# Optimization experiments

Measured on AMD Instinct MI355X. Metric: run time of the kernel, lower is better.

## Reference

```python
import jax, jax.numpy as jnp
import numpy as np
import math

N_HEADS = 8

def _layernorm(x, s, b):
    mu = x.mean(-1, keepdims=True)
    var = ((x - mu) ** 2).mean(-1, keepdims=True)
    return (x - mu) / jnp.sqrt(var + 1e-5) * s + b


def setup_inputs() -> dict:
    key = jax.random.key(0)
    ks = jax.random.split(key, 16)
    B, S, F, E, L, C, DFF = 4, 2048, 16, 512, 4, 35, 2048
    feat = jax.random.normal(ks[0], (B, S, F - 1), dtype=jnp.float32)
    amino = jax.random.randint(ks[1], (B, S), 0, 20).astype(jnp.float32)
    x = jnp.concatenate([feat, amino[..., None]], axis=-1)  # last channel = amino id
    lengths = np.array([2048, 1900, 1700, 1500])
    mask = jnp.asarray(np.arange(S)[None, :] >= lengths[:, None])  # True = padding
    M = 256
    rng = np.random.default_rng(0)
    mp = np.stack([np.sort(rng.choice(int(lengths[b]) - 1, M, replace=False)) for b in range(B)])
    masked_pos = jnp.asarray(mp, dtype=jnp.int32)
    # sinusoidal positional encoding [S, E]
    pos = np.arange(S)[:, None].astype(np.float32)
    div = np.exp(np.arange(0, E, 2).astype(np.float32) * (-math.log(10000.0) / E))
    pe_np = np.zeros((S, E), np.float32)
    pe_np[:, 0::2] = np.sin(pos * div)
    pe_np[:, 1::2] = np.cos(pos * div)
    pe = jnp.asarray(pe_np)
    sc = 1.0 / math.sqrt(E)
    def w(k, shape, s=sc):
        return jax.random.normal(k, shape, dtype=jnp.float32) * s
    return dict(
        x=x, mask=mask, masked_pos=masked_pos,
        arg1=jnp.float32(0.5), arg2=jnp.float32(0.8),
        embed_table=w(ks[2], (20, E - 15), 1.0), pe=pe,
        Wq=w(ks[3], (L, E, E)), bq=jnp.zeros((L, E)),
        Wk=w(ks[4], (L, E, E)), bk=jnp.zeros((L, E)),
        Wv=w(ks[5], (L, E, E)), bv=jnp.zeros((L, E)),
        Wo=w(ks[6], (L, E, E)), bo=jnp.zeros((L, E)),
        ln1_s=jnp.ones((L, E)), ln1_b=jnp.zeros((L, E)),
        W1=w(ks[7], (L, E, DFF)), b1=jnp.zeros((L, DFF)),
        W2=w(ks[8], (L, DFF, E), 1.0 / math.sqrt(DFF)), b2=jnp.zeros((L, E)),
        ln2_s=jnp.ones((L, E)), ln2_b=jnp.zeros((L, E)),
        fc_w=w(ks[9], (E, C)), fc_b=jnp.zeros((C,)),
    )


def _forward(x, mask, masked_pos, arg1, arg2, embed_table, pe, Wq, bq, Wk, bk, Wv, bv,
             Wo, bo, ln1_s, ln1_b, W1, b1, W2, b2, ln2_s, ln2_b, fc_w, fc_b):
    B, S, F = x.shape
    E = pe.shape[1]
    L = Wq.shape[0]
    H = N_HEADS
    Dh = E // H
    bidx = jnp.arange(B)[:, None]
    # get_mask: zero the masked token rows; label = original rows at masked positions
    mask_x = x.at[bidx, masked_pos].set(0.0)
    label = x[bidx, masked_pos].reshape(-1, F)
    # amino embedding with per-token min-max normalization
    amino = mask_x[:, :, -1].astype(jnp.int32)
    emb = embed_table[amino]  # [B,S,E-15]
    mn = emb.min(-1, keepdims=True)
    mx = emb.max(-1, keepdims=True)
    emb = (emb - mn) / (mx - mn)
    h = jnp.concatenate([mask_x[:, :, :-1], emb], axis=-1) + pe[None, :S, :]
    base = (~mask).astype(jnp.float32)  # 1 = valid key, 0 = pad
    for i in range(L):
        fill = arg1 if i == 0 else (arg2 if i == 1 else jnp.float32(1.0))
        m = base.at[bidx, masked_pos].set(fill)  # [B,S] key weights
        q = (h @ Wq[i] + bq[i]).reshape(B, S, H, Dh).transpose(0, 2, 1, 3)
        k = (h @ Wk[i] + bk[i]).reshape(B, S, H, Dh).transpose(0, 2, 1, 3)
        v = (h @ Wv[i] + bv[i]).reshape(B, S, H, Dh).transpose(0, 2, 1, 3)
        scores = jnp.einsum('bhqd,bhkd->bhqk', q, k) / Dh  # note: /head_dim, not sqrt
        mvec = m[:, None, None, :]
        scores = jnp.where(mvec != 0, scores * mvec, -jnp.inf)
        attn = jax.nn.softmax(scores, axis=-1)
        ws = jnp.einsum('bhqk,bhkd->bhqd', attn, v)  # [B,H,S,Dh]
        # faithful to torch: stacked [B,H,S,Dh].view(B,-1,E) row-major flatten
        attn_out = ws.reshape(B, -1, E) @ Wo[i] + bo[i]
        h = _layernorm(h + attn_out, ln1_s[i], ln1_b[i])
        ff = jax.nn.relu(h @ W1[i] + b1[i]) @ W2[i] + b2[i]
        h = _layernorm(h + ff, ln2_s[i], ln2_b[i])
    out_tok = h[bidx, masked_pos].reshape(-1, E)
    output = out_tok @ fc_w + fc_b
    return output[:, :15], output[:, 15:], label, h


def reference(x, mask, masked_pos, arg1, arg2, embed_table, pe, Wq, bq, Wk, bk, Wv, bv,
              Wo, bo, ln1_s, ln1_b, W1, b1, W2, b2, ln2_s, ln2_b, fc_w, fc_b):
    L1, CE, label, h = _forward(x, mask, masked_pos, arg1, arg2, embed_table, pe, Wq, bq,
                                Wk, bk, Wv, bv, Wo, bo, ln1_s, ln1_b, W1, b1, W2, b2,
                                ln2_s, ln2_b, fc_w, fc_b)
    return (L1, CE, label, h, mask)
```

## Files before the change

### kernel.cpp

```cpp
#include <hip/hip_runtime.h>
#include <hip/hip_bf16.h>


typedef __bf16 bf16_t;
typedef __bf16 bf16x8 __attribute__((ext_vector_type(8)));
typedef __bf16 bf16x4 __attribute__((ext_vector_type(4)));
typedef float  f32x4  __attribute__((ext_vector_type(4)));

#define ASYNC16(g, l) __builtin_amdgcn_global_load_lds( \
    (const __attribute__((address_space(1))) void*)(g),  \
    (__attribute__((address_space(3))) void*)(l), 16, 0, 0)

static __device__ __forceinline__ f32x4 mfma16(bf16x8 a, bf16x8 b, f32x4 c) {
  return __builtin_amdgcn_mfma_f32_16x16x32_bf16(a, b, c, 0, 0, 0);
}

static __device__ __forceinline__ float fexp2(float x) {
#if __has_builtin(__builtin_amdgcn_exp2f)
  return __builtin_amdgcn_exp2f(x);
#else
  return exp2f(x);
#endif
}

#define L2E 1.44269504f

__global__ void zero_flags_k(int* __restrict__ flags) {
  flags[blockIdx.x * 256 + threadIdx.x] = 0;
}

__global__ void scatter_k(const int* __restrict__ mpos, int* __restrict__ flags) {
  int t = blockIdx.x * 256 + threadIdx.x;
  int b = t >> 8;
  flags[b * 2048 + mpos[t]] = 1;
}

__global__ void masks_k(const int* __restrict__ flags,
                        const float* __restrict__ a1, const float* __restrict__ a2,
                        float* __restrict__ m05, float* __restrict__ m08,
                        float* __restrict__ mbase, float* __restrict__ maskout) {
  int i = blockIdx.x * 256 + threadIdx.x;
  int b = i >> 11, s = i & 2047;
  const int len0 = (b == 0) ? 2048 : (b == 1) ? 1900 : (b == 2) ? 1700 : 1500;
  float bs = (s < len0) ? 1.f : 0.f;
  int fl = flags[i];
  m05[i]   = fl ? a1[0] : bs;
  m08[i]   = fl ? a2[0] : bs;
  mbase[i] = fl ? 1.f   : bs;
  maskout[i] = 1.f - bs;
}

__global__ void label_k(const float* __restrict__ x, const int* __restrict__ mpos,
                        float* __restrict__ out) {
  int idx = blockIdx.x * 256 + threadIdx.x;
  int t = idx >> 4, f = idx & 15;
  int b = t >> 8;
  int pos = mpos[t];
  out[idx] = x[(b * 2048 + pos) * 16 + f];
}

__global__ __launch_bounds__(512) void embed_k(
    const float* __restrict__ x, const int* __restrict__ flags,
    const float* __restrict__ et, const float* __restrict__ pe,
    float* __restrict__ hf, bf16_t* __restrict__ hb) {
  const int tok = blockIdx.x, tid = threadIdx.x;
  const int s = tok & 2047;
  const int wave = tid >> 6, lane = tid & 63;
  __shared__ float e[512];
  __shared__ float redn[8], redx[8];
  const int masked = flags[tok];
  const float amf = masked ? 0.f : x[tok * 16 + 15];
  const int am = (int)amf;
  float ev = 0.f, vn = 3e38f, vx = -3e38f;
  if (tid < 497) { ev = et[am * 497 + tid]; e[tid] = ev; vn = ev; vx = ev; }
#pragma unroll
  for (int off = 1; off < 64; off <<= 1) {
    vn = fminf(vn, __shfl_xor(vn, off, 64));
    vx = fmaxf(vx, __shfl_xor(vx, off, 64));
  }
  if (lane == 0) { redn[wave] = vn; redx[wave] = vx; }
  __syncthreads();
  float mn = redn[0], mx = redx[0];
#pragma unroll
  for (int w = 1; w < 8; ++w) { mn = fminf(mn, redn[w]); mx = fmaxf(mx, redx[w]); }
  float val;
  if (tid < 15) val = masked ? 0.f : x[tok * 16 + tid];
  else          val = (e[tid - 15] - mn) / (mx - mn);
  val += pe[s * 512 + tid];
  hf[(size_t)tok * 512 + tid] = val;
  hb[(size_t)tok * 512 + tid] = (bf16_t)val;
}

__global__ void transpose_k(const float* __restrict__ in, bf16_t* __restrict__ out,
                            int K, int N, size_t ozstride) {
  __shared__ float t[32][33];
  in  += (size_t)blockIdx.z * K * N;
  out += (size_t)blockIdx.z * ozstride;
  const int n0 = blockIdx.x * 32, k0 = blockIdx.y * 32;
  const int tx = threadIdx.x & 31, ty = threadIdx.x >> 5;
#pragma unroll
  for (int i = 0; i < 32; i += 8)
    t[ty + i][tx] = in[(size_t)(k0 + ty + i) * N + n0 + tx];
  __syncthreads();
#pragma unroll
  for (int i = 0; i < 32; i += 8)
    out[(size_t)(n0 + ty + i) * K + k0 + tx] = (bf16_t)t[tx][ty + i];
}

template <int EPI>
__global__ __launch_bounds__(256) void gemm_k(
    const bf16_t* __restrict__ A, const bf16_t* __restrict__ Bt,
    const float* __restrict__ bias, const float* __restrict__ resid,
    float* __restrict__ outf, bf16_t* __restrict__ outb,
    int M, int N, int K) {
  __shared__ alignas(16) bf16_t As[2][128 * 32];
  __shared__ alignas(16) bf16_t Bs[2][128 * 32];
  const int tid = threadIdx.x;
  const int wave = tid >> 6, lane = tid & 63;
  const int quad = lane >> 4, l16 = lane & 15;
  const int n0 = blockIdx.x * 128, m0 = blockIdx.y * 128;
  const int wm = (wave & 1) * 64, wn = (wave >> 1) * 64;

  const int c0 = wave * 2, c1 = c0 + 1;
  const int sr = lane >> 2;
  const int sc = (((lane & 3) ^ ((sr >> 1) & 3))) * 8;
  const bf16_t* Ag0 = A + (size_t)(m0 + c0 * 16 + sr) * K + sc;
  const bf16_t* Ag1 = A + (size_t)(m0 + c1 * 16 + sr) * K + sc;
  const bf16_t* Bg0 = Bt + (size_t)(n0 + c0 * 16 + sr) * K + sc;
  const bf16_t* Bg1 = Bt + (size_t)(n0 + c1 * 16 + sr) * K + sc;

  const int cq = (quad ^ ((l16 >> 1) & 3)) * 8;

  f32x4 acc[4][4] = {};
  const int nit = K >> 5;

  ASYNC16(Ag0, &As[0][c0 * 512]);
  ASYNC16(Ag1, &As[0][c1 * 512]);
  ASYNC16(Bg0, &Bs[0][c0 * 512]);
  ASYNC16(Bg1, &Bs[0][c1 * 512]);
  __syncthreads();

  for (int it = 0; it < nit; ++it) {
    const int cur = it & 1, nxt = cur ^ 1;
    if (it + 1 < nit) {
      const int ko = (it + 1) << 5;
      ASYNC16(Ag0 + ko, &As[nxt][c0 * 512]);
      ASYNC16(Ag1 + ko, &As[nxt][c1 * 512]);
      ASYNC16(Bg0 + ko, &Bs[nxt][c0 * 512]);
      ASYNC16(Bg1 + ko, &Bs[nxt][c1 * 512]);
    }
    bf16x8 af[4], bfr[4];
#pragma unroll
    for (int mi = 0; mi < 4; ++mi)
      af[mi] = *(const bf16x8*)&As[cur][(wm + mi * 16 + l16) * 32 + cq];
#pragma unroll
    for (int ni = 0; ni < 4; ++ni)
      bfr[ni] = *(const bf16x8*)&Bs[cur][(wn + ni * 16 + l16) * 32 + cq];
#pragma unroll
    for (int mi = 0; mi < 4; ++mi)
#pragma unroll
      for (int ni = 0; ni < 4; ++ni)
        acc[mi][ni] = mfma16(af[mi], bfr[ni], acc[mi][ni]);
    __syncthreads();
  }

#pragma unroll
  for (int ni = 0; ni < 4; ++ni) {
    const int gn = n0 + wn + ni * 16 + l16;
    const float bv = bias[gn];
#pragma unroll
    for (int mi = 0; mi < 4; ++mi) {
#pragma unroll
      for (int r = 0; r < 4; ++r) {
        const int gm = m0 + wm + mi * 16 + quad * 4 + r;
        float v = acc[mi][ni][r] + bv;
        if (EPI == 2) {
          outf[(size_t)gm * N + gn] = v + resid[(size_t)gm * N + gn];
        } else {
          outb[(size_t)gm * N + gn] = (bf16_t)fmaxf(v, 0.f);
        }
      }
    }
  }
}

__global__ __launch_bounds__(256) void gemm64_k(
    const bf16_t* __restrict__ A, const bf16_t* __restrict__ Bt,
    const float* __restrict__ bias, const float* __restrict__ resid,
    float* __restrict__ outf, int M, int N, int K) {
  __shared__ alignas(16) bf16_t As[2][64 * 64];
  __shared__ alignas(16) bf16_t Bs[2][128 * 64];
  const int tid = threadIdx.x;
  const int wave = tid >> 6, lane = tid & 63;
  const int quad = lane >> 4, l16 = lane & 15;
  const int n0 = blockIdx.x * 128, m0 = blockIdx.y * 64;
  const int wm = (wave & 1) * 32, wn = (wave >> 1) * 64;

  const bf16_t* gptr[6];
  int soff[6];
  bool isA[6];
#pragma unroll
  for (int i = 0; i < 6; ++i) {
    const int s = tid + 256 * i;
    if (s < 512) {
      const int r = s >> 3, c = s & 7, g = c ^ ((r >> 1) & 7);
      gptr[i] = A + (size_t)(m0 + r) * K + g * 8;
      soff[i] = s * 16;  isA[i] = true;
    } else {
      const int sb = s - 512;
      const int r = sb >> 3, c = sb & 7, g = c ^ ((r >> 1) & 7);
      gptr[i] = Bt + (size_t)(n0 + r) * K + g * 8;
      soff[i] = sb * 16; isA[i] = false;
    }
  }

  const int swl = (l16 >> 1) & 7;
  f32x4 acc[2][4] = {};
  const int nit = K >> 6;

#pragma unroll
  for (int i = 0; i < 6; ++i)
    ASYNC16(gptr[i], (char*)(isA[i] ? &As[0][0] : &Bs[0][0]) + soff[i]);
  __syncthreads();

  for (int it = 0; it < nit; ++it) {
    const int cur = it & 1, nxt = cur ^ 1;
    if (it + 1 < nit) {
      const int ko = (it + 1) << 6;
#pragma unroll
      for (int i = 0; i < 6; ++i)
        ASYNC16(gptr[i] + ko, (char*)(isA[i] ? &As[nxt][0] : &Bs[nxt][0]) + soff[i]);
    }
#pragma unroll
    for (int h = 0; h < 2; ++h) {
      const int cq = ((quad + 4 * h) ^ swl) * 8;
      bf16x8 af[2], bfr[4];
#pragma unroll
      for (int mi = 0; mi < 2; ++mi)
        af[mi] = *(const bf16x8*)&As[cur][(wm + mi * 16 + l16) * 64 + cq];
#pragma unroll
      for (int ni = 0; ni < 4; ++ni)
        bfr[ni] = *(const bf16x8*)&Bs[cur][(wn + ni * 16 + l16) * 64 + cq];
#pragma unroll
      for (int mi = 0; mi < 2; ++mi)
#pragma unroll
        for (int ni = 0; ni < 4; ++ni)
          acc[mi][ni] = mfma16(af[mi], bfr[ni], acc[mi][ni]);
    }
    __syncthreads();
  }

#pragma unroll
  for (int ni = 0; ni < 4; ++ni) {
    const int gn = n0 + wn + ni * 16 + l16;
    const float bv = bias[gn];
#pragma unroll
    for (int mi = 0; mi < 2; ++mi) {
#pragma unroll
      for (int r = 0; r < 4; ++r) {
        const int gm = m0 + wm + mi * 16 + quad * 4 + r;
        outf[(size_t)gm * N + gn] = acc[mi][ni][r] + bv + resid[(size_t)gm * N + gn];
      }
    }
  }
}

__global__ __launch_bounds__(256) void gemm_qkv_k(
    const bf16_t* __restrict__ A, const bf16_t* __restrict__ Bt,
    const float* __restrict__ bq, const float* __restrict__ bk,
    const float* __restrict__ bv, const float* __restrict__ mw,
    bf16_t* __restrict__ qb, bf16_t* __restrict__ kb, bf16_t* __restrict__ vtb) {
  const int K = 512;
  __shared__ alignas(16) bf16_t As[2][128 * 32];
  __shared__ alignas(16) bf16_t Bs[2][128 * 32];
  const int tid = threadIdx.x;
  const int wave = tid >> 6, lane = tid & 63;
  const int quad = lane >> 4, l16 = lane & 15;
  const int n0 = blockIdx.x * 128, m0 = blockIdx.y * 128;
  const int wm = (wave & 1) * 64, wn = (wave >> 1) * 64;

  const int c0 = wave * 2, c1 = c0 + 1;
  const int sr = lane >> 2;
  const int sc = (((lane & 3) ^ ((sr >> 1) & 3))) * 8;
  const bf16_t* Ag0 = A + (size_t)(m0 + c0 * 16 + sr) * K + sc;
  const bf16_t* Ag1 = A + (size_t)(m0 + c1 * 16 + sr) * K + sc;
  const bf16_t* Bg0 = Bt + (size_t)(n0 + c0 * 16 + sr) * K + sc;
  const bf16_t* Bg1 = Bt + (size_t)(n0 + c1 * 16 + sr) * K + sc;

  const int cq = (quad ^ ((l16 >> 1) & 3)) * 8;

  f32x4 acc[4][4] = {};
  const int nit = K >> 5;

  ASYNC16(Ag0, &As[0][c0 * 512]);
  ASYNC16(Ag1, &As[0][c1 * 512]);
  ASYNC16(Bg0, &Bs[0][c0 * 512]);
  ASYNC16(Bg1, &Bs[0][c1 * 512]);
  __syncthreads();

  for (int it = 0; it < nit; ++it) {
    const int cur = it & 1, nxt = cur ^ 1;
    if (it + 1 < nit) {
      const int ko = (it + 1) << 5;
      ASYNC16(Ag0 + ko, &As[nxt][c0 * 512]);
      ASYNC16(Ag1 + ko, &As[nxt][c1 * 512]);
      ASYNC16(Bg0 + ko, &Bs[nxt][c0 * 512]);
      ASYNC16(Bg1 + ko, &Bs[nxt][c1 * 512]);
    }
    bf16x8 af[4], bfr[4];
#pragma unroll
    for (int mi = 0; mi < 4; ++mi)
      af[mi] = *(const bf16x8*)&As[cur][(wm + mi * 16 + l16) * 32 + cq];
#pragma unroll
    for (int ni = 0; ni < 4; ++ni)
      bfr[ni] = *(const bf16x8*)&Bs[cur][(wn + ni * 16 + l16) * 32 + cq];
#pragma unroll
    for (int mi = 0; mi < 4; ++mi)
#pragma unroll
      for (int ni = 0; ni < 4; ++ni)
        acc[mi][ni] = mfma16(af[mi], bfr[ni], acc[mi][ni]);
    __syncthreads();
  }

  const int which = n0 >> 9;
  const float* bias = (which == 0) ? bq : (which == 1) ? bk : bv;
  bf16_t* dst = (which == 0) ? qb : (which == 1) ? kb : vtb;
  float kmul[4][4];
  if (which == 1) {
#pragma unroll
    for (int mi = 0; mi < 4; ++mi)
#pragma unroll
      for (int r = 0; r < 4; ++r) {
        const int gm = m0 + wm + mi * 16 + quad * 4 + r;
        kmul[mi][r] = mw[(gm >> 11) * 2048 + (gm & 2047)] * (0.015625f * L2E);
      }
  }
#pragma unroll
  for (int ni = 0; ni < 4; ++ni) {
    const int gn = n0 + wn + ni * 16 + l16;
    const int col = gn & 511;
    const float bvx = bias[col];
    const int hh = col >> 6, dd = col & 63;
#pragma unroll
    for (int mi = 0; mi < 4; ++mi) {
#pragma unroll
      for (int r = 0; r < 4; ++r) {
        const int gm = m0 + wm + mi * 16 + quad * 4 + r;
        const int bb = gm >> 11, ss = gm & 2047;
        float v = acc[mi][ni][r] + bvx;
        if (which == 0) {
          dst[(size_t)(((bb * 8 + hh) * 2048) + ss) * 64 + dd] = (bf16_t)v;
        } else if (which == 1) {
          v *= kmul[mi][r];
          dst[(size_t)(((bb * 8 + hh) * 2048) + ss) * 64 + dd] = (bf16_t)v;
        } else {
          const int o5 = ss & 31;
          const int ssp = (ss & ~31) | ((o5 & 12) << 1) | ((o5 & 16) >> 2) | (o5 & 3);
          dst[(size_t)(((bb * 8 + hh) * 64) + dd) * 2048 + ssp] = (bf16_t)v;
        }
      }
    }
  }
}

__global__ __launch_bounds__(256, 2) void attn_k(
    const bf16_t* __restrict__ Q, const bf16_t* __restrict__ Kmat,
    const bf16_t* __restrict__ VT, bf16_t* __restrict__ out) {
  __shared__ alignas(16) bf16_t Ks[128 * 64];
  __shared__ alignas(16) bf16_t Vs[64 * 128];
  const int tid = threadIdx.x, wave = tid >> 6, lane = tid & 63;
  const int quad = lane >> 4, l16 = lane & 15;
  const int qt = blockIdx.x, bh = blockIdx.y;
  const int b = bh >> 3, hh = bh & 7;
  const int len = (b == 0) ? 2048 : (b == 1) ? 1900 : (b == 2) ? 1700 : 1500;
  const bf16_t* __restrict__ Qh = Q    + (size_t)bh * 2048 * 64;
  const bf16_t* __restrict__ Kh = Kmat + (size_t)bh * 2048 * 64;
  const bf16_t* __restrict__ Vh = VT   + (size_t)bh * 64 * 2048;
  const int q0 = qt * 128 + wave * 32;

  bf16x8 aq[2][2];
#pragma unroll
  for (int qf = 0; qf < 2; ++qf) {
    aq[qf][0] = *(const bf16x8*)&Qh[(size_t)(q0 + qf * 16 + l16) * 64 + quad * 8];
    aq[qf][1] = *(const bf16x8*)&Qh[(size_t)(q0 + qf * 16 + l16) * 64 + 32 + quad * 8];
  }

  f32x4 o[2][4] = {};
  f32x4 os[2] = {};
  bf16x8 onesb;
#pragma unroll
  for (int j = 0; j < 8; ++j) onesb[j] = (bf16_t)1.0f;

  const int krow = wave * 8 + (lane >> 3);
  const int kchk = (lane & 7) ^ (lane >> 3);
  const int vrow = wave * 4 + (lane >> 4);
  const int vchk = (lane & 15) ^ (wave * 4 + (lane >> 4));
  const int kc0 = quad ^ (l16 & 7);
  const int kc1 = (quad + 4) ^ (l16 & 7);

  const int ntiles = (len + 127) >> 7;
  for (int kt = 0; kt < ntiles; ++kt) {
    const int k0 = kt * 128;
    __syncthreads();
#pragma unroll
    for (int i = 0; i < 4; ++i)
      ASYNC16(Kh + (size_t)(k0 + i * 32 + krow) * 64 + kchk * 8,
              &Ks[(i * 32 + wave * 8) * 64]);
#pragma unroll
    for (int i = 0; i < 4; ++i)
      ASYNC16(Vh + (size_t)(i * 16 + vrow) * 2048 + k0 + vchk * 8,
              &Vs[(i * 16 + wave * 4) * 128]);
    __syncthreads();

    f32x4 sc0[8], sc1[8];
#pragma unroll
    for (int t = 0; t < 8; ++t) {
      const bf16x8 kf0 = *(const bf16x8*)&Ks[(t * 16 + l16) * 64 + kc0 * 8];
      const bf16x8 kf1 = *(const bf16x8*)&Ks[(t * 16 + l16) * 64 + kc1 * 8];
      f32x4 z0 = {0.f, 0.f, 0.f, 0.f};
      z0 = mfma16(kf0, aq[0][0], z0);
      z0 = mfma16(kf1, aq[0][1], z0);
      sc0[t] = z0;
      f32x4 z1 = {0.f, 0.f, 0.f, 0.f};
      z1 = mfma16(kf0, aq[1][0], z1);
      z1 = mfma16(kf1, aq[1][1], z1);
      sc1[t] = z1;
    }
    if (k0 + 128 > len) {
#pragma unroll
      for (int t = 0; t < 8; ++t)
#pragma unroll
        for (int r = 0; r < 4; ++r) {
          const bool pad = (k0 + t * 16 + quad * 4 + r >= len);
          if (pad) { sc0[t][r] = -1e30f; sc1[t][r] = -1e30f; }
        }
    }
    bf16x8 pbp[2][4];
#pragma unroll
    for (int t = 0; t < 8; ++t)
#pragma unroll
      for (int r = 0; r < 4; ++r) {
        pbp[0][t >> 1][(t & 1) * 4 + r] = (bf16_t)fexp2(sc0[t][r]);
        pbp[1][t >> 1][(t & 1) * 4 + r] = (bf16_t)fexp2(sc1[t][r]);
      }
#pragma unroll
    for (int T = 0; T < 4; ++T) {
      const int slot = ((4 * T + quad) ^ l16) * 8;
#pragma unroll
      for (int ni = 0; ni < 4; ++ni) {
        const bf16x8 vb = *(const bf16x8*)&Vs[(ni * 16 + l16) * 128 + slot];
        o[0][ni] = mfma16(pbp[0][T], vb, o[0][ni]);
        o[1][ni] = mfma16(pbp[1][T], vb, o[1][ni]);
      }
      os[0] = mfma16(pbp[0][T], onesb, os[0]);
      os[1] = mfma16(pbp[1][T], onesb, os[1]);
    }
  }

#pragma unroll
  for (int qf = 0; qf < 2; ++qf) {
    float linv[4];
#pragma unroll
    for (int r = 0; r < 4; ++r) linv[r] = 1.f / os[qf][r];
#pragma unroll
    for (int ni = 0; ni < 4; ++ni) {
#pragma unroll
      for (int r = 0; r < 4; ++r) {
        const int s_tok = q0 + qf * 16 + quad * 4 + r;
        const int d = ni * 16 + l16;
        const int row = b * 2048 + hh * 256 + (s_tok >> 3);
        const int col = (s_tok & 7) * 64 + d;
        out[(size_t)row * 512 + col] = (bf16_t)(o[qf][ni][r] * linv[r]);
      }
    }
  }
}

__global__ __launch_bounds__(256) void ln_k(
    const float* __restrict__ in, const float* __restrict__ sc,
    const float* __restrict__ bi, float* __restrict__ hf, bf16_t* __restrict__ hb) {
  const int row = blockIdx.x, tid = threadIdx.x;
  const int wave = tid >> 6, lane = tid & 63;
  const float* x = in + (size_t)row * 512;
  float v0 = x[tid], v1 = x[tid + 256];
  float s = v0 + v1, s2 = v0 * v0 + v1 * v1;
#pragma unroll
  for (int off = 1; off < 64; off <<= 1) {
    s  += __shfl_xor(s, off, 64);
    s2 += __shfl_xor(s2, off, 64);
  }
  __shared__ float red[8];
  if (lane == 0) { red[wave] = s; red[4 + wave] = s2; }
  __syncthreads();
  float ts  = red[0] + red[1] + red[2] + red[3];
  float ts2 = red[4] + red[5] + red[6] + red[7];
  float mu = ts * (1.f / 512.f);
  float var = ts2 * (1.f / 512.f) - mu * mu;
  float rstd = rsqrtf(var + 1e-5f);
  float o0 = (v0 - mu) * rstd * sc[tid] + bi[tid];
  float o1 = (v1 - mu) * rstd * sc[tid + 256] + bi[tid + 256];
  hf[(size_t)row * 512 + tid] = o0;
  hf[(size_t)row * 512 + tid + 256] = o1;
  hb[(size_t)row * 512 + tid] = (bf16_t)o0;
  hb[(size_t)row * 512 + tid + 256] = (bf16_t)o1;
}

__global__ void head_k(const float* __restrict__ hf, const int* __restrict__ mpos,
                       const float* __restrict__ fw, const float* __restrict__ fb,
                       float* __restrict__ out0, float* __restrict__ out1) {
  const int t = blockIdx.x;
  const int b = t >> 8;
  const int pos = mpos[t];
  const float* hr = hf + (size_t)(b * 2048 + pos) * 512;
  __shared__ float hrow[512];
  for (int i = threadIdx.x; i < 512; i += 64) hrow[i] = hr[i];
  __syncthreads();
  const int c = threadIdx.x;
  if (c < 35) {
    float acc = fb[c];
    for (int k = 0; k < 512; ++k) acc += hrow[k] * fw[k * 35 + c];
    if (c < 15) out0[t * 15 + c] = acc;
    else        out1[t * 20 + (c - 15)] = acc;
  }
}

extern "C" void kernel_launch(void* const* d_in, const int* in_sizes, int n_in,
                              void* d_out, int out_size, void* d_ws, size_t ws_size,
                              hipStream_t stream) {
  const float* x    = (const float*)d_in[0];
  const int*   mpos = (const int*)d_in[2];
  const float* a1   = (const float*)d_in[3];
  const float* a2   = (const float*)d_in[4];
  const float* et   = (const float*)d_in[5];
  const float* pe   = (const float*)d_in[6];
  const float* Wq   = (const float*)d_in[7];
  const float* bq   = (const float*)d_in[8];
  const float* Wk   = (const float*)d_in[9];
  const float* bk   = (const float*)d_in[10];
  const float* Wv   = (const float*)d_in[11];
  const float* bv   = (const float*)d_in[12];
  const float* Wo   = (const float*)d_in[13];
  const float* bo   = (const float*)d_in[14];
  const float* l1s  = (const float*)d_in[15];
  const float* l1b  = (const float*)d_in[16];
  const float* W1   = (const float*)d_in[17];
  const float* b1   = (const float*)d_in[18];
  const float* W2   = (const float*)d_in[19];
  const float* b2   = (const float*)d_in[20];
  const float* l2s  = (const float*)d_in[21];
  const float* l2b  = (const float*)d_in[22];
  const float* fcw  = (const float*)d_in[23];
  const float* fcb  = (const float*)d_in[24];

  char* w = (char*)d_ws;
  const size_t MB = 1024 * 1024;
  bf16_t* qkvT = (bf16_t*)(w + 0 * MB);
  bf16_t* wot  = (bf16_t*)(w + 6 * MB);
  bf16_t* w1t  = (bf16_t*)(w + 8 * MB);
  bf16_t* w2t  = (bf16_t*)(w + 16 * MB);
  float*  hf   = (float*) (w + 24 * MB);
  bf16_t* hb   = (bf16_t*)(w + 40 * MB);
  float*  tmp  = (float*) (w + 48 * MB);
  int*    flags= (int*)   (w + 64 * MB);
  float*  m05  = (float*) (w + 64 * MB + 64 * 1024);
  float*  m08  = (float*) (w + 64 * MB + 128 * 1024);
  float*  mba  = (float*) (w + 64 * MB + 192 * 1024);
  bf16_t* qb   = (bf16_t*)(w + 65 * MB);
  bf16_t* kb   = (bf16_t*)(w + 73 * MB);
  bf16_t* vtb  = (bf16_t*)(w + 81 * MB);
  bf16_t* ao   = (bf16_t*)(w + 89 * MB);
  bf16_t* ff1  = (bf16_t*)(w + 65 * MB);

  float* out0    = (float*)d_out;
  float* out1    = out0 + 1024 * 15;
  float* outlab  = out1 + 1024 * 20;
  float* outh    = outlab + 1024 * 16;
  float* outmask = outh + 4 * 2048 * 512;

  zero_flags_k<<<32, 256, 0, stream>>>(flags);
  scatter_k<<<4, 256, 0, stream>>>(mpos, flags);
  masks_k<<<32, 256, 0, stream>>>(flags, a1, a2, m05, m08, mba, outmask);
  embed_k<<<8192, 512, 0, stream>>>(x, flags, et, pe, hf, hb);
  label_k<<<64, 256, 0, stream>>>(x, mpos, outlab);
  transpose_k<<<dim3(16, 16, 4), 256, 0, stream>>>(Wq, qkvT + 0 * 262144, 512, 512, 786432);
  transpose_k<<<dim3(16, 16, 4), 256, 0, stream>>>(Wk, qkvT + 1 * 262144, 512, 512, 786432);
  transpose_k<<<dim3(16, 16, 4), 256, 0, stream>>>(Wv, qkvT + 2 * 262144, 512, 512, 786432);
  transpose_k<<<dim3(16, 16, 4), 256, 0, stream>>>(Wo, wot, 512, 512, 262144);
  transpose_k<<<dim3(64, 16, 4), 256, 0, stream>>>(W1, w1t, 512, 2048, 1048576);
  transpose_k<<<dim3(16, 64, 4), 256, 0, stream>>>(W2, w2t, 2048, 512, 1048576);

  for (int i = 0; i < 4; ++i) {
    const float* mv = (i == 0) ? m05 : (i == 1) ? m08 : mba;
    gemm_qkv_k<<<dim3(12, 64), 256, 0, stream>>>(hb, qkvT + (size_t)i * 786432,
                                                 bq + i * 512, bk + i * 512, bv + i * 512,
                                                 mv, qb, kb, vtb);
    attn_k<<<dim3(16, 32), 256, 0, stream>>>(qb, kb, vtb, ao);
    gemm64_k<<<dim3(4, 128), 256, 0, stream>>>(ao, wot + i * 262144, bo + i * 512,
                                               hf, tmp, 8192, 512, 512);
    ln_k<<<8192, 256, 0, stream>>>(tmp, l1s + i * 512, l1b + i * 512, hf, hb);
    gemm_k<3><<<dim3(16, 64), 256, 0, stream>>>(hb, w1t + i * 1048576, b1 + i * 2048,
                                                nullptr, nullptr, ff1, 8192, 2048, 512);
    gemm64_k<<<dim3(4, 128), 256, 0, stream>>>(ff1, w2t + i * 1048576, b2 + i * 512,
                                               hf, tmp, 8192, 512, 2048);
    float* lnout = (i == 3) ? outh : hf;
    ln_k<<<8192, 256, 0, stream>>>(tmp, l2s + i * 512, l2b + i * 512, lnout, hb);
  }
  head_k<<<1024, 64, 0, stream>>>(outh, mpos, fcw, fcb, out0, out1);
}
```

Baseline: 874.6 us.

## Keep residual stream in bf16, double-buffer attention K/V, widen QKV k-tile

The fp32 hidden-state copy is removed: residual adds and layernorm inputs and outputs now use bf16 buffers, and only the final layer writes fp32 output. This cuts memory traffic in the gemm epilogues and layernorm. The attention kernel now double-buffers K/V tiles so the next tile loads while the current one computes, the QKV GEMM uses a 64-wide k-tile, and the four weight transposes are merged into one launch. Keeping the residual in bf16 lowers accuracy, and the larger shared-memory footprint in attention may reduce occupancy.

```diff
diff --git a/kernel.cpp b/kernel.cpp
--- a/kernel.cpp
+++ b/kernel.cpp
@@ -4,12 +4,15 @@
 
 typedef __bf16 bf16_t;
 typedef __bf16 bf16x8 __attribute__((ext_vector_type(8)));
-typedef __bf16 bf16x4 __attribute__((ext_vector_type(4)));
+typedef __bf16 bf16x2 __attribute__((ext_vector_type(2)));
 typedef float  f32x4  __attribute__((ext_vector_type(4)));
 
 #define ASYNC16(g, l) __builtin_amdgcn_global_load_lds( \
     (const __attribute__((address_space(1))) void*)(g),  \
     (__attribute__((address_space(3))) void*)(l), 16, 0, 0)
+
+#define S_VMCNT0() asm volatile("s_waitcnt vmcnt(0)" ::: "memory")
+#define S_BARRIER() asm volatile("s_barrier" ::: "memory")
 
 static __device__ __forceinline__ f32x4 mfma16(bf16x8 a, bf16x8 b, f32x4 c) {
   return __builtin_amdgcn_mfma_f32_16x16x32_bf16(a, b, c, 0, 0, 0);
@@ -62,7 +65,7 @@
 __global__ __launch_bounds__(512) void embed_k(
     const float* __restrict__ x, const int* __restrict__ flags,
     const float* __restrict__ et, const float* __restrict__ pe,
-    float* __restrict__ hf, bf16_t* __restrict__ hb) {
+    bf16_t* __restrict__ hb) {
   const int tok = blockIdx.x, tid = threadIdx.x;
   const int s = tok & 2047;
   const int wave = tid >> 6, lane = tid & 63;
@@ -87,7 +90,6 @@
   if (tid < 15) val = masked ? 0.f : x[tok * 16 + tid];
   else          val = (e[tid - 15] - mn) / (mx - mn);
   val += pe[s * 512 + tid];
-  hf[(size_t)tok * 512 + tid] = val;
   hb[(size_t)tok * 512 + tid] = (bf16_t)val;
 }
 
@@ -107,11 +109,30 @@
     out[(size_t)(n0 + ty + i) * K + k0 + tx] = (bf16_t)t[tx][ty + i];
 }
 
+__global__ void transpose4_k(const float* __restrict__ Wq, const float* __restrict__ Wk,
+                             const float* __restrict__ Wv, const float* __restrict__ Wo,
+                             bf16_t* __restrict__ qkvT, bf16_t* __restrict__ wot) {
+  __shared__ float t[32][33];
+  const int z = blockIdx.z, l = z >> 2, f = z & 3;
+  const float* in = ((f == 0) ? Wq : (f == 1) ? Wk : (f == 2) ? Wv : Wo)
+                    + (size_t)l * 262144;
+  bf16_t* out = (f < 3) ? qkvT + (size_t)l * 786432 + (size_t)f * 262144
+                        : wot + (size_t)l * 262144;
+  const int n0 = blockIdx.x * 32, k0 = blockIdx.y * 32;
+  const int tx = threadIdx.x & 31, ty = threadIdx.x >> 5;
+#pragma unroll
+  for (int i = 0; i < 32; i += 8)
+    t[ty + i][tx] = in[(size_t)(k0 + ty + i) * 512 + n0 + tx];
+  __syncthreads();
+#pragma unroll
+  for (int i = 0; i < 32; i += 8)
+    out[(size_t)(n0 + ty + i) * 512 + k0 + tx] = (bf16_t)t[tx][ty + i];
+}
+
 template <int EPI>
 __global__ __launch_bounds__(256) void gemm_k(
     const bf16_t* __restrict__ A, const bf16_t* __restrict__ Bt,
-    const float* __restrict__ bias, const float* __restrict__ resid,
-    float* __restrict__ outf, bf16_t* __restrict__ outb,
+    const float* __restrict__ bias, bf16_t* __restrict__ outb,
     int M, int N, int K) {
   __shared__ alignas(16) bf16_t As[2][128 * 32];
   __shared__ alignas(16) bf16_t Bs[2][128 * 32];
@@ -173,12 +194,8 @@
 #pragma unroll
       for (int r = 0; r < 4; ++r) {
         const int gm = m0 + wm + mi * 16 + quad * 4 + r;
-        float v = acc[mi][ni][r] + bv;
-        if (EPI == 2) {
-          outf[(size_t)gm * N + gn] = v + resid[(size_t)gm * N + gn];
-        } else {
-          outb[(size_t)gm * N + gn] = (bf16_t)fmaxf(v, 0.f);
-        }
+        const float v = acc[mi][ni][r] + bv;
+        outb[(size_t)gm * N + gn] = (bf16_t)fmaxf(v, 0.f);
       }
     }
   }
@@ -186,8 +203,8 @@
 
 __global__ __launch_bounds__(256) void gemm64_k(
     const bf16_t* __restrict__ A, const bf16_t* __restrict__ Bt,
-    const float* __restrict__ bias, const float* __restrict__ resid,
-    float* __restrict__ outf, int M, int N, int K) {
+    const float* __restrict__ bias, const bf16_t* __restrict__ residb,
+    bf16_t* __restrict__ outb, int M, int N, int K) {
   __shared__ alignas(16) bf16_t As[2][64 * 64];
   __shared__ alignas(16) bf16_t Bs[2][128 * 64];
   const int tid = threadIdx.x;
@@ -259,7 +276,8 @@
 #pragma unroll
       for (int r = 0; r < 4; ++r) {
         const int gm = m0 + wm + mi * 16 + quad * 4 + r;
-        outf[(size_t)gm * N + gn] = acc[mi][ni][r] + bv + resid[(size_t)gm * N + gn];
+        const float v = acc[mi][ni][r] + bv + (float)residb[(size_t)gm * N + gn];
+        outb[(size_t)gm * N + gn] = (bf16_t)v;
       }
     }
   }
@@ -271,54 +289,65 @@
     const float* __restrict__ bv, const float* __restrict__ mw,
     bf16_t* __restrict__ qb, bf16_t* __restrict__ kb, bf16_t* __restrict__ vtb) {
   const int K = 512;
-  __shared__ alignas(16) bf16_t As[2][128 * 32];
-  __shared__ alignas(16) bf16_t Bs[2][128 * 32];
+  __shared__ alignas(16) bf16_t As[2][128 * 64];
+  __shared__ alignas(16) bf16_t Bs[2][128 * 64];
   const int tid = threadIdx.x;
   const int wave = tid >> 6, lane = tid & 63;
   const int quad = lane >> 4, l16 = lane & 15;
   const int n0 = blockIdx.x * 128, m0 = blockIdx.y * 128;
   const int wm = (wave & 1) * 64, wn = (wave >> 1) * 64;
 
-  const int c0 = wave * 2, c1 = c0 + 1;
-  const int sr = lane >> 2;
-  const int sc = (((lane & 3) ^ ((sr >> 1) & 3))) * 8;
-  const bf16_t* Ag0 = A + (size_t)(m0 + c0 * 16 + sr) * K + sc;
-  const bf16_t* Ag1 = A + (size_t)(m0 + c1 * 16 + sr) * K + sc;
-  const bf16_t* Bg0 = Bt + (size_t)(n0 + c0 * 16 + sr) * K + sc;
-  const bf16_t* Bg1 = Bt + (size_t)(n0 + c1 * 16 + sr) * K + sc;
-
-  const int cq = (quad ^ ((l16 >> 1) & 3)) * 8;
+  const bf16_t* gp[8];
+  int soff[8];
+  bool ia[8];
+#pragma unroll
+  for (int i = 0; i < 8; ++i) {
+    const int s = tid + 256 * i;
+    if (s < 1024) {
+      const int r = s >> 3, c = s & 7, g = c ^ ((r >> 1) & 7);
+      gp[i] = A + (size_t)(m0 + r) * K + g * 8;
+      soff[i] = s * 16; ia[i] = true;
+    } else {
+      const int sb = s - 1024;
+      const int r = sb >> 3, c = sb & 7, g = c ^ ((r >> 1) & 7);
+      gp[i] = Bt + (size_t)(n0 + r) * K + g * 8;
+      soff[i] = sb * 16; ia[i] = false;
+    }
+  }
+  const int swl = (l16 >> 1) & 7;
 
   f32x4 acc[4][4] = {};
-  const int nit = K >> 5;
-
-  ASYNC16(Ag0, &As[0][c0 * 512]);
-  ASYNC16(Ag1, &As[0][c1 * 512]);
-  ASYNC16(Bg0, &Bs[0][c0 * 512]);
-  ASYNC16(Bg1, &Bs[0][c1 * 512]);
+  const int nit = K >> 6;
+
+#pragma unroll
+  for (int i = 0; i < 8; ++i)
+    ASYNC16(gp[i], (char*)(ia[i] ? &As[0][0] : &Bs[0][0]) + soff[i]);
   __syncthreads();
 
   for (int it = 0; it < nit; ++it) {
     const int cur = it & 1, nxt = cur ^ 1;
     if (it + 1 < nit) {
-      const int ko = (it + 1) << 5;
-      ASYNC16(Ag0 + ko, &As[nxt][c0 * 512]);
-      ASYNC16(Ag1 + ko, &As[nxt][c1 * 512]);
-      ASYNC16(Bg0 + ko, &Bs[nxt][c0 * 512]);
-      ASYNC16(Bg1 + ko, &Bs[nxt][c1 * 512]);
-    }
-    bf16x8 af[4], bfr[4];
-#pragma unroll
-    for (int mi = 0; mi < 4; ++mi)
-      af[mi] = *(const bf16x8*)&As[cur][(wm + mi * 16 + l16) * 32 + cq];
-#pragma unroll
-    for (int ni = 0; ni < 4; ++ni)
-      bfr[ni] = *(const bf16x8*)&Bs[cur][(wn + ni * 16 + l16) * 32 + cq];
-#pragma unroll
-    for (int mi = 0; mi < 4; ++mi)
+      const int ko = (it + 1) << 6;
+#pragma unroll
+      for (int i = 0; i < 8; ++i)
+        ASYNC16(gp[i] + ko, (char*)(ia[i] ? &As[nxt][0] : &Bs[nxt][0]) + soff[i]);
+    }
+#pragma unroll
+    for (int h = 0; h < 2; ++h) {
+      const int cq = ((quad + 4 * h) ^ swl) * 8;
+      bf16x8 af[4], bfr[4];
+#pragma unroll
+      for (int mi = 0; mi < 4; ++mi)
+        af[mi] = *(const bf16x8*)&As[cur][(wm + mi * 16 + l16) * 64 + cq];
 #pragma unroll
       for (int ni = 0; ni < 4; ++ni)
-        acc[mi][ni] = mfma16(af[mi], bfr[ni], acc[mi][ni]);
+        bfr[ni] = *(const bf16x8*)&Bs[cur][(wn + ni * 16 + l16) * 64 + cq];
+#pragma unroll
+      for (int mi = 0; mi < 4; ++mi)
+#pragma unroll
+        for (int ni = 0; ni < 4; ++ni)
+          acc[mi][ni] = mfma16(af[mi], bfr[ni], acc[mi][ni]);
+    }
     __syncthreads();
   }
 
@@ -366,8 +395,8 @@
 __global__ __launch_bounds__(256, 2) void attn_k(
     const bf16_t* __restrict__ Q, const bf16_t* __restrict__ Kmat,
     const bf16_t* __restrict__ VT, bf16_t* __restrict__ out) {
-  __shared__ alignas(16) bf16_t Ks[128 * 64];
-  __shared__ alignas(16) bf16_t Vs[64 * 128];
+  __shared__ alignas(16) bf16_t Ks[2][128 * 64];
+  __shared__ alignas(16) bf16_t Vs[2][64 * 128];
   const int tid = threadIdx.x, wave = tid >> 6, lane = tid & 63;
   const int quad = lane >> 4, l16 = lane & 15;
   const int qt = blockIdx.x, bh = blockIdx.y;
@@ -399,24 +428,39 @@
   const int kc1 = (quad + 4) ^ (l16 & 7);
 
   const int ntiles = (len + 127) >> 7;
+
+#pragma unroll
+  for (int i = 0; i < 4; ++i)
+    ASYNC16(Kh + (size_t)(i * 32 + krow) * 64 + kchk * 8,
+            &Ks[0][(i * 32 + wave * 8) * 64]);
+#pragma unroll
+  for (int i = 0; i < 4; ++i)
+    ASYNC16(Vh + (size_t)(i * 16 + vrow) * 2048 + vchk * 8,
+            &Vs[0][(i * 16 + wave * 4) * 128]);
+
   for (int kt = 0; kt < ntiles; ++kt) {
+    S_VMCNT0();
+    S_BARRIER();
+    if (kt + 1 < ntiles) {
+      const int k1 = (kt + 1) * 128;
+      const int nb = (kt + 1) & 1;
+#pragma unroll
+      for (int i = 0; i < 4; ++i)
+        ASYNC16(Kh + (size_t)(k1 + i * 32 + krow) * 64 + kchk * 8,
+                &Ks[nb][(i * 32 + wave * 8) * 64]);
+#pragma unroll
+      for (int i = 0; i < 4; ++i)
+        ASYNC16(Vh + (size_t)(i * 16 + vrow) * 2048 + k1 + vchk * 8,
+                &Vs[nb][(i * 16 + wave * 4) * 128]);
+    }
+    const int cb = kt & 1;
     const int k0 = kt * 128;
-    __syncthreads();
-#pragma unroll
-    for (int i = 0; i < 4; ++i)
-      ASYNC16(Kh + (size_t)(k0 + i * 32 + krow) * 64 + kchk * 8,
-              &Ks[(i * 32 + wave * 8) * 64]);
-#pragma unroll
-    for (int i = 0; i < 4; ++i)
-      ASYNC16(Vh + (size_t)(i * 16 + vrow) * 2048 + k0 + vchk * 8,
-              &Vs[(i * 16 + wave * 4) * 128]);
-    __syncthreads();
 
     f32x4 sc0[8], sc1[8];
 #pragma unroll
     for (int t = 0; t < 8; ++t) {
-      const bf16x8 kf0 = *(const bf16x8*)&Ks[(t * 16 + l16) * 64 + kc0 * 8];
-      const bf16x8 kf1 = *(const bf16x8*)&Ks[(t * 16 + l16) * 64 + kc1 * 8];
+      const bf16x8 kf0 = *(const bf16x8*)&Ks[cb][(t * 16 + l16) * 64 + kc0 * 8];
+      const bf16x8 kf1 = *(const bf16x8*)&Ks[cb][(t * 16 + l16) * 64 + kc1 * 8];
       f32x4 z0 = {0.f, 0.f, 0.f, 0.f};
       z0 = mfma16(kf0, aq[0][0], z0);
       z0 = mfma16(kf1, aq[0][1], z0);
@@ -448,7 +492,7 @@
       const int slot = ((4 * T + quad) ^ l16) * 8;
 #pragma unroll
       for (int ni = 0; ni < 4; ++ni) {
-        const bf16x8 vb = *(const bf16x8*)&Vs[(ni * 16 + l16) * 128 + slot];
+        const bf16x8 vb = *(const bf16x8*)&Vs[cb][(ni * 16 + l16) * 128 + slot];
         o[0][ni] = mfma16(pbp[0][T], vb, o[0][ni]);
         o[1][ni] = mfma16(pbp[1][T], vb, o[1][ni]);
       }
@@ -477,12 +521,13 @@
 }
 
 __global__ __launch_bounds__(256) void ln_k(
-    const float* __restrict__ in, const float* __restrict__ sc,
-    const float* __restrict__ bi, float* __restrict__ hf, bf16_t* __restrict__ hb) {
+    const bf16_t* __restrict__ in, const float* __restrict__ sc,
+    const float* __restrict__ bi, bf16_t* __restrict__ hb,
+    float* __restrict__ outf) {
   const int row = blockIdx.x, tid = threadIdx.x;
   const int wave = tid >> 6, lane = tid & 63;
-  const float* x = in + (size_t)row * 512;
-  float v0 = x[tid], v1 = x[tid + 256];
+  const bf16x2 v2 = ((const bf16x2*)(in + (size_t)row * 512))[tid];
+  const float v0 = (float)v2[0], v1 = (float)v2[1];
   float s = v0 + v1, s2 = v0 * v0 + v1 * v1;
 #pragma unroll
   for (int off = 1; off < 64; off <<= 1) {
@@ -497,12 +542,15 @@
   float mu = ts * (1.f / 512.f);
   float var = ts2 * (1.f / 512.f) - mu * mu;
   float rstd = rsqrtf(var + 1e-5f);
-  float o0 = (v0 - mu) * rstd * sc[tid] + bi[tid];
-  float o1 = (v1 - mu) * rstd * sc[tid + 256] + bi[tid + 256];
-  hf[(size_t)row * 512 + tid] = o0;
-  hf[(size_t)row * 512 + tid + 256] = o1;
-  hb[(size_t)row * 512 + tid] = (bf16_t)o0;
-  hb[(size_t)row * 512 + tid + 256] = (bf16_t)o1;
+  const int c0 = tid * 2, c1 = c0 + 1;
+  float o0 = (v0 - mu) * rstd * sc[c0] + bi[c0];
+  float o1 = (v1 - mu) * rstd * sc[c1] + bi[c1];
+  bf16x2 ob; ob[0] = (bf16_t)o0; ob[1] = (bf16_t)o1;
+  ((bf16x2*)(hb + (size_t)row * 512))[tid] = ob;
+  if (outf) {
+    outf[(size_t)row * 512 + c0] = o0;
+    outf[(size_t)row * 512 + c1] = o1;
+  }
 }
 
 __global__ void head_k(const float* __restrict__ hf, const int* __restrict__ mpos,
@@ -558,18 +606,17 @@
   bf16_t* wot  = (bf16_t*)(w + 6 * MB);
   bf16_t* w1t  = (bf16_t*)(w + 8 * MB);
   bf16_t* w2t  = (bf16_t*)(w + 16 * MB);
-  float*  hf   = (float*) (w + 24 * MB);
-  bf16_t* hb   = (bf16_t*)(w + 40 * MB);
-  float*  tmp  = (float*) (w + 48 * MB);
-  int*    flags= (int*)   (w + 64 * MB);
-  float*  m05  = (float*) (w + 64 * MB + 64 * 1024);
-  float*  m08  = (float*) (w + 64 * MB + 128 * 1024);
-  float*  mba  = (float*) (w + 64 * MB + 192 * 1024);
-  bf16_t* qb   = (bf16_t*)(w + 65 * MB);
-  bf16_t* kb   = (bf16_t*)(w + 73 * MB);
-  bf16_t* vtb  = (bf16_t*)(w + 81 * MB);
-  bf16_t* ao   = (bf16_t*)(w + 89 * MB);
-  bf16_t* ff1  = (bf16_t*)(w + 65 * MB);
+  bf16_t* hb   = (bf16_t*)(w + 24 * MB);
+  bf16_t* tmpb = (bf16_t*)(w + 32 * MB);
+  int*    flags= (int*)   (w + 40 * MB);
+  float*  m05  = (float*) (w + 40 * MB + 64 * 1024);
+  float*  m08  = (float*) (w + 40 * MB + 128 * 1024);
+  float*  mba  = (float*) (w + 40 * MB + 192 * 1024);
+  bf16_t* qb   = (bf16_t*)(w + 41 * MB);
+  bf16_t* kb   = (bf16_t*)(w + 49 * MB);
+  bf16_t* vtb  = (bf16_t*)(w + 57 * MB);
+  bf16_t* ao   = (bf16_t*)(w + 65 * MB);
+  bf16_t* ff1  = (bf16_t*)(w + 73 * MB);
 
   float* out0    = (float*)d_out;
   float* out1    = out0 + 1024 * 15;
@@ -580,12 +627,9 @@
   zero_flags_k<<<32, 256, 0, stream>>>(flags);
   scatter_k<<<4, 256, 0, stream>>>(mpos, flags);
   masks_k<<<32, 256, 0, stream>>>(flags, a1, a2, m05, m08, mba, outmask);
-  embed_k<<<8192, 512, 0, stream>>>(x, flags, et, pe, hf, hb);
+  embed_k<<<8192, 512, 0, stream>>>(x, flags, et, pe, hb);
   label_k<<<64, 256, 0, stream>>>(x, mpos, outlab);
-  transpose_k<<<dim3(16, 16, 4), 256, 0, stream>>>(Wq, qkvT + 0 * 262144, 512, 512, 786432);
-  transpose_k<<<dim3(16, 16, 4), 256, 0, stream>>>(Wk, qkvT + 1 * 262144, 512, 512, 786432);
-  transpose_k<<<dim3(16, 16, 4), 256, 0, stream>>>(Wv, qkvT + 2 * 262144, 512, 512, 786432);
-  transpose_k<<<dim3(16, 16, 4), 256, 0, stream>>>(Wo, wot, 512, 512, 262144);
+  transpose4_k<<<dim3(16, 16, 16), 256, 0, stream>>>(Wq, Wk, Wv, Wo, qkvT, wot);
   transpose_k<<<dim3(64, 16, 4), 256, 0, stream>>>(W1, w1t, 512, 2048, 1048576);
   transpose_k<<<dim3(16, 64, 4), 256, 0, stream>>>(W2, w2t, 2048, 512, 1048576);
 
@@ -596,14 +640,14 @@
                                                  mv, qb, kb, vtb);
     attn_k<<<dim3(16, 32), 256, 0, stream>>>(qb, kb, vtb, ao);
     gemm64_k<<<dim3(4, 128), 256, 0, stream>>>(ao, wot + i * 262144, bo + i * 512,
-                                               hf, tmp, 8192, 512, 512);
-    ln_k<<<8192, 256, 0, stream>>>(tmp, l1s + i * 512, l1b + i * 512, hf, hb);
+                                               hb, tmpb, 8192, 512, 512);
+    ln_k<<<8192, 256, 0, stream>>>(tmpb, l1s + i * 512, l1b + i * 512, hb, nullptr);
     gemm_k<3><<<dim3(16, 64), 256, 0, stream>>>(hb, w1t + i * 1048576, b1 + i * 2048,
-                                                nullptr, nullptr, ff1, 8192, 2048, 512);
+                                                ff1, 8192, 2048, 512);
     gemm64_k<<<dim3(4, 128), 256, 0, stream>>>(ff1, w2t + i * 1048576, b2 + i * 512,
-                                               hf, tmp, 8192, 512, 2048);
-    float* lnout = (i == 3) ? outh : hf;
-    ln_k<<<8192, 256, 0, stream>>>(tmp, l2s + i * 512, l2b + i * 512, lnout, hb);
+                                               hb, tmpb, 8192, 512, 2048);
+    ln_k<<<8192, 256, 0, stream>>>(tmpb, l2s + i * 512, l2b + i * 512, hb,
+                                   (i == 3) ? outh : nullptr);
   }
   head_k<<<1024, 64, 0, stream>>>(outh, mpos, fcw, fcb, out0, out1);
 }
```

After: 880.6 us. About the same (+0.7%).
